# Kernel optimization log

Measured on AMD Instinct MI355X. Metric: run time of the kernel, lower is better.

## Reference

```python
import jax, jax.numpy as jnp
import numpy as np

NENTITY = 100000
NRELATION = 500
HIDDEN = 256
GAMMA = 12.0
BATCH = 8


def setup_inputs() -> dict:
    key = jax.random.key(0)
    k1, k2, k3, k4 = jax.random.split(key, 4)
    entity_embedding = jax.random.normal(k1, (NENTITY, HIDDEN), dtype=jnp.float32)
    relation_embedding = jax.random.normal(k2, (NRELATION, HIDDEN), dtype=jnp.float32)
    positive_sample = jax.random.randint(k3, (BATCH, 3), 0, NRELATION, dtype=jnp.int64)
    negative_sample = jax.random.randint(k4, (BATCH, NENTITY), 0, NENTITY, dtype=jnp.int64)
    return {
        "entity_embedding": entity_embedding,
        "relation_embedding": relation_embedding,
        "positive_sample": positive_sample,
        "negative_sample": negative_sample,
    }


def reference(entity_embedding, relation_embedding, positive_sample, negative_sample):
    # 'tail-batch' mode of KGEModel.forward + TransE scoring.
    # head, relation come from the positive triple; tail is every negative candidate.
    head = entity_embedding[positive_sample[:, 0]][:, None, :]      # [B, 1, H]
    relation = relation_embedding[positive_sample[:, 1]][:, None, :]  # [B, 1, H]
    tail = entity_embedding[negative_sample]                          # [B, N, H]
    # score = gamma - || head + relation - tail ||_1
    score = GAMMA - jnp.sum(jnp.abs(head + relation - tail), axis=-1)  # [B, N]
    return score
```

## Files before the change

kernel.cpp:

```cpp
#include <hip/hip_runtime.h>

#define HIDDEN 256
#define GAMMA_F 12.0f
#define BATCH 8

__global__ __launch_bounds__(256) void kge_dist_kernel(
    const float* __restrict__ ent,
    const float* __restrict__ rel,
    const int*  __restrict__ pos,
    float* __restrict__ dist,
    int ngroups, int nent)
{
    const int lane = threadIdx.x & 63;
    const int r = lane >> 5;
    const int c = lane & 31;
    const int wave_gid = (blockIdx.x * 256 + threadIdx.x) >> 6;
    const int nwaves = gridDim.x * 4;

    float4 hrA[BATCH], hrB[BATCH];
    #pragma unroll
    for (int b = 0; b < BATCH; ++b) {
        const int hidx = pos[b * 3 + 0];
        const int ridx = pos[b * 3 + 1];
        const float* hrow = ent + (size_t)hidx * HIDDEN;
        const float* rrow = rel + (size_t)ridx * HIDDEN;
        float4 h = *(const float4*)(hrow + c * 4);
        float4 q = *(const float4*)(rrow + c * 4);
        hrA[b] = make_float4(h.x + q.x, h.y + q.y, h.z + q.z, h.w + q.w);
        h = *(const float4*)(hrow + 128 + c * 4);
        q = *(const float4*)(rrow + 128 + c * 4);
        hrB[b] = make_float4(h.x + q.x, h.y + q.y, h.z + q.z, h.w + q.w);
    }

    for (int grp = wave_gid; grp < ngroups; grp += nwaves) {
        const float* base = ent + (size_t)grp * 8 * HIDDEN;

        float4 tA[4], tB[4];
        #pragma unroll
        for (int j = 0; j < 4; ++j) {
            const float* rowb = base + (size_t)(2 * j + r) * HIDDEN;
            tA[j] = *(const float4*)(rowb + c * 4);
            tB[j] = *(const float4*)(rowb + 128 + c * 4);
        }

        float res = 0.0f;
        #pragma unroll
        for (int j = 0; j < 4; ++j) {
            float acc[BATCH];
            #pragma unroll
            for (int b = 0; b < BATCH; ++b) {
                acc[b] = fabsf(hrA[b].x - tA[j].x) + fabsf(hrA[b].y - tA[j].y)
                       + fabsf(hrA[b].z - tA[j].z) + fabsf(hrA[b].w - tA[j].w)
                       + fabsf(hrB[b].x - tB[j].x) + fabsf(hrB[b].y - tB[j].y)
                       + fabsf(hrB[b].z - tB[j].z) + fabsf(hrB[b].w - tB[j].w);
            }
            float v[4];
            {
                const bool p = lane & 1;
                #pragma unroll
                for (int k = 0; k < 4; ++k) {
                    const float keep = p ? acc[2 * k + 1] : acc[2 * k];
                    const float give = p ? acc[2 * k]     : acc[2 * k + 1];
                    v[k] = keep + __shfl_xor(give, 1, 64);
                }
            }
            float w2[2];
            {
                const bool p = (lane >> 1) & 1;
                #pragma unroll
                for (int k = 0; k < 2; ++k) {
                    const float keep = p ? v[2 * k + 1] : v[2 * k];
                    const float give = p ? v[2 * k]     : v[2 * k + 1];
                    w2[k] = keep + __shfl_xor(give, 2, 64);
                }
            }
            float s;
            {
                const bool p = (lane >> 2) & 1;
                const float keep = p ? w2[1] : w2[0];
                const float give = p ? w2[0] : w2[1];
                s = keep + __shfl_xor(give, 4, 64);
            }
            s += __shfl_xor(s, 8, 64);
            s += __shfl_xor(s, 16, 64);
            if (((lane >> 3) & 3) == j) res = GAMMA_F - s;
        }
        dist[(size_t)grp * 64 + ((lane >> 3) & 3) * 16 + r * 8 + (lane & 7)] = res;
    }

    if (wave_gid == 0) {
        for (int e = ngroups * 8; e < nent; ++e) {
            const float* rowb = ent + (size_t)e * HIDDEN;
            const float4 uA = *(const float4*)(rowb + c * 4);
            const float4 uB = *(const float4*)(rowb + 128 + c * 4);
            float acc[BATCH];
            #pragma unroll
            for (int b = 0; b < BATCH; ++b) {
                acc[b] = fabsf(hrA[b].x - uA.x) + fabsf(hrA[b].y - uA.y)
                       + fabsf(hrA[b].z - uA.z) + fabsf(hrA[b].w - uA.w)
                       + fabsf(hrB[b].x - uB.x) + fabsf(hrB[b].y - uB.y)
                       + fabsf(hrB[b].z - uB.z) + fabsf(hrB[b].w - uB.w);
            }
            float v[4];
            {
                const bool p = lane & 1;
                #pragma unroll
                for (int k = 0; k < 4; ++k) {
                    const float keep = p ? acc[2 * k + 1] : acc[2 * k];
                    const float give = p ? acc[2 * k]     : acc[2 * k + 1];
                    v[k] = keep + __shfl_xor(give, 1, 64);
                }
            }
            float w2[2];
            {
                const bool p = (lane >> 1) & 1;
                #pragma unroll
                for (int k = 0; k < 2; ++k) {
                    const float keep = p ? v[2 * k + 1] : v[2 * k];
                    const float give = p ? v[2 * k]     : v[2 * k + 1];
                    w2[k] = keep + __shfl_xor(give, 2, 64);
                }
            }
            float s;
            {
                const bool p = (lane >> 2) & 1;
                const float keep = p ? w2[1] : w2[0];
                const float give = p ? w2[0] : w2[1];
                s = keep + __shfl_xor(give, 4, 64);
            }
            s += __shfl_xor(s, 8, 64);
            s += __shfl_xor(s, 16, 64);
            if (lane < BATCH) dist[(size_t)e * BATCH + lane] = GAMMA_F - s;
        }
    }
}

__global__ __launch_bounds__(256) void kge_gather_kernel(
    const int*  __restrict__ neg,
    const float* __restrict__ dist,
    float* __restrict__ out,
    int nneg)
{
    const int b = blockIdx.y;
    const int n = (blockIdx.x * 256 + threadIdx.x) * 2;
    if (n + 1 < nneg) {
        const int2 idx = *(const int2*)(neg + (size_t)b * nneg + n);
        float2 r;
        r.x = dist[(size_t)idx.x * BATCH + b];
        r.y = dist[(size_t)idx.y * BATCH + b];
        *(float2*)(out + (size_t)b * nneg + n) = r;
    } else if (n < nneg) {
        out[(size_t)b * nneg + n] =
            dist[(size_t)neg[(size_t)b * nneg + n] * BATCH + b];
    }
}

extern "C" void kernel_launch(void* const* d_in, const int* in_sizes, int n_in,
                              void* d_out, int out_size, void* d_ws, size_t ws_size,
                              hipStream_t stream) {
    const float* ent = (const float*)d_in[0];
    const float* rel = (const float*)d_in[1];
    const int*   pos = (const int*)d_in[2];
    const int*   neg = (const int*)d_in[3];
    float* out = (float*)d_out;

    const int nent = in_sizes[0] / HIDDEN;
    const int nneg = in_sizes[3] / BATCH;
    float* dist = (float*)d_ws;

    const int ngroups = nent / 8;
    kge_dist_kernel<<<1024, 256, 0, stream>>>(ent, rel, pos, dist, ngroups, nent);

    const int npairs = (nneg + 1) / 2;
    dim3 gridB((npairs + 255) / 256, BATCH);
    kge_gather_kernel<<<gridB, 256, 0, stream>>>(neg, dist, out, nneg);
}
```

Baseline: 166.0 us.

## Double-buffer entity rows into LDS via direct global-to-LDS loads per wave

Replaces direct register loads of 8-row entity groups with per-wave double-buffered LDS staging of 4-row groups using global_load_lds, prefetching the next group while computing the current one. The goal is to hide global memory latency on the full entity-table stream. The change halves the group size, adds manual waitcnt management and 32KB of LDS per block, and relies on each wave reading only its own LDS slot without barriers.

```diff
diff --git a/kernel.cpp b/kernel.cpp
--- a/kernel.cpp
+++ b/kernel.cpp
@@ -3,19 +3,33 @@
 #define HIDDEN 256
 #define GAMMA_F 12.0f
 #define BATCH 8
-
-__global__ __launch_bounds__(256) void kge_dist_kernel(
+#define ROWS_PER_GRP 4
+#define GRP_FLOATS (ROWS_PER_GRP * HIDDEN)
+
+__device__ __forceinline__ void dma_row_16(const float* gsrc, float* ldst) {
+    __builtin_amdgcn_global_load_lds(
+        (const __attribute__((address_space(1))) unsigned int*)gsrc,
+        (__attribute__((address_space(3))) unsigned int*)ldst,
+        16, 0, 0);
+}
+
+#define WAITCNT_VM4 0xF74
+#define WAITCNT_VM0 0xF70
+
+__global__ __launch_bounds__(256, 4) void kge_dist_kernel(
     const float* __restrict__ ent,
     const float* __restrict__ rel,
     const int*  __restrict__ pos,
     float* __restrict__ dist,
-    int ngroups, int nent)
+    int ngroups, int nent, int nwaves)
 {
+    __shared__ float lds[4][2][GRP_FLOATS];
+
     const int lane = threadIdx.x & 63;
-    const int r = lane >> 5;
+    const int wslot = threadIdx.x >> 6;
+    const int r_ = lane >> 5;
     const int c = lane & 31;
     const int wave_gid = (blockIdx.x * 256 + threadIdx.x) >> 6;
-    const int nwaves = gridDim.x * 4;
 
     float4 hrA[BATCH], hrB[BATCH];
     #pragma unroll
@@ -32,64 +46,85 @@
         hrB[b] = make_float4(h.x + q.x, h.y + q.y, h.z + q.z, h.w + q.w);
     }
 
-    for (int grp = wave_gid; grp < ngroups; grp += nwaves) {
-        const float* base = ent + (size_t)grp * 8 * HIDDEN;
-
-        float4 tA[4], tB[4];
+    __builtin_amdgcn_s_waitcnt(WAITCNT_VM0);
+
+    int g = wave_gid;
+    int p = 0;
+    if (g < ngroups) {
+        const float* base = ent + (size_t)g * GRP_FLOATS;
         #pragma unroll
-        for (int j = 0; j < 4; ++j) {
-            const float* rowb = base + (size_t)(2 * j + r) * HIDDEN;
-            tA[j] = *(const float4*)(rowb + c * 4);
-            tB[j] = *(const float4*)(rowb + 128 + c * 4);
+        for (int rr = 0; rr < ROWS_PER_GRP; ++rr)
+            dma_row_16(base + rr * HIDDEN + lane * 4, &lds[wslot][0][rr * HIDDEN]);
+    }
+
+    while (g < ngroups) {
+        const int gn = g + nwaves;
+        if (gn < ngroups) {
+            const float* base = ent + (size_t)gn * GRP_FLOATS;
+            #pragma unroll
+            for (int rr = 0; rr < ROWS_PER_GRP; ++rr)
+                dma_row_16(base + rr * HIDDEN + lane * 4,
+                           &lds[wslot][p ^ 1][rr * HIDDEN]);
+            __builtin_amdgcn_s_waitcnt(WAITCNT_VM4);
+        } else {
+            __builtin_amdgcn_s_waitcnt(WAITCNT_VM0);
         }
 
+        const float* buf = &lds[wslot][p][0];
         float res = 0.0f;
+        const int q = (lane >> 3) & 3;
         #pragma unroll
-        for (int j = 0; j < 4; ++j) {
+        for (int j = 0; j < 2; ++j) {
+            const float4 tA = *(const float4*)(buf + (2 * j + r_) * HIDDEN + c * 4);
+            const float4 tB = *(const float4*)(buf + (2 * j + r_) * HIDDEN + 128 + c * 4);
             float acc[BATCH];
             #pragma unroll
             for (int b = 0; b < BATCH; ++b) {
-                acc[b] = fabsf(hrA[b].x - tA[j].x) + fabsf(hrA[b].y - tA[j].y)
-                       + fabsf(hrA[b].z - tA[j].z) + fabsf(hrA[b].w - tA[j].w)
-                       + fabsf(hrB[b].x - tB[j].x) + fabsf(hrB[b].y - tB[j].y)
-                       + fabsf(hrB[b].z - tB[j].z) + fabsf(hrB[b].w - tB[j].w);
+                acc[b] = fabsf(hrA[b].x - tA.x) + fabsf(hrA[b].y - tA.y)
+                       + fabsf(hrA[b].z - tA.z) + fabsf(hrA[b].w - tA.w)
+                       + fabsf(hrB[b].x - tB.x) + fabsf(hrB[b].y - tB.y)
+                       + fabsf(hrB[b].z - tB.z) + fabsf(hrB[b].w - tB.w);
             }
             float v[4];
             {
-                const bool p = lane & 1;
+                const bool pb = lane & 1;
                 #pragma unroll
                 for (int k = 0; k < 4; ++k) {
-                    const float keep = p ? acc[2 * k + 1] : acc[2 * k];
-                    const float give = p ? acc[2 * k]     : acc[2 * k + 1];
+                    const float keep = pb ? acc[2 * k + 1] : acc[2 * k];
+                    const float give = pb ? acc[2 * k]     : acc[2 * k + 1];
                     v[k] = keep + __shfl_xor(give, 1, 64);
                 }
             }
             float w2[2];
             {
-                const bool p = (lane >> 1) & 1;
+                const bool pb = (lane >> 1) & 1;
                 #pragma unroll
                 for (int k = 0; k < 2; ++k) {
-                    const float keep = p ? v[2 * k + 1] : v[2 * k];
-                    const float give = p ? v[2 * k]     : v[2 * k + 1];
+                    const float keep = pb ? v[2 * k + 1] : v[2 * k];
+                    const float give = pb ? v[2 * k]     : v[2 * k + 1];
                     w2[k] = keep + __shfl_xor(give, 2, 64);
                 }
             }
             float s;
             {
-                const bool p = (lane >> 2) & 1;
-                const float keep = p ? w2[1] : w2[0];
-                const float give = p ? w2[0] : w2[1];
+                const bool pb = (lane >> 2) & 1;
+                const float keep = pb ? w2[1] : w2[0];
+                const float give = pb ? w2[0] : w2[1];
                 s = keep + __shfl_xor(give, 4, 64);
             }
             s += __shfl_xor(s, 8, 64);
             s += __shfl_xor(s, 16, 64);
-            if (((lane >> 3) & 3) == j) res = GAMMA_F - s;
+            if (q == j) res = GAMMA_F - s;
         }
-        dist[(size_t)grp * 64 + ((lane >> 3) & 3) * 16 + r * 8 + (lane & 7)] = res;
+        if (q < 2)
+            dist[(size_t)g * (ROWS_PER_GRP * BATCH) + q * 16 + r_ * 8 + (lane & 7)] = res;
+
+        p ^= 1;
+        g = gn;
     }
 
     if (wave_gid == 0) {
-        for (int e = ngroups * 8; e < nent; ++e) {
+        for (int e = ngroups * ROWS_PER_GRP; e < nent; ++e) {
             const float* rowb = ent + (size_t)e * HIDDEN;
             const float4 uA = *(const float4*)(rowb + c * 4);
             const float4 uB = *(const float4*)(rowb + 128 + c * 4);
@@ -103,29 +138,29 @@
             }
             float v[4];
             {
-                const bool p = lane & 1;
+                const bool pb = lane & 1;
                 #pragma unroll
                 for (int k = 0; k < 4; ++k) {
-                    const float keep = p ? acc[2 * k + 1] : acc[2 * k];
-                    const float give = p ? acc[2 * k]     : acc[2 * k + 1];
+                    const float keep = pb ? acc[2 * k + 1] : acc[2 * k];
+                    const float give = pb ? acc[2 * k]     : acc[2 * k + 1];
                     v[k] = keep + __shfl_xor(give, 1, 64);
                 }
             }
             float w2[2];
             {
-                const bool p = (lane >> 1) & 1;
+                const bool pb = (lane >> 1) & 1;
                 #pragma unroll
                 for (int k = 0; k < 2; ++k) {
-                    const float keep = p ? v[2 * k + 1] : v[2 * k];
-                    const float give = p ? v[2 * k]     : v[2 * k + 1];
+                    const float keep = pb ? v[2 * k + 1] : v[2 * k];
+                    const float give = pb ? v[2 * k]     : v[2 * k + 1];
                     w2[k] = keep + __shfl_xor(give, 2, 64);
                 }
             }
             float s;
             {
-                const bool p = (lane >> 2) & 1;
-                const float keep = p ? w2[1] : w2[0];
-                const float give = p ? w2[0] : w2[1];
+                const bool pb = (lane >> 2) & 1;
+                const float keep = pb ? w2[1] : w2[0];
+                const float give = pb ? w2[0] : w2[1];
                 s = keep + __shfl_xor(give, 4, 64);
             }
             s += __shfl_xor(s, 8, 64);
@@ -168,8 +203,11 @@
     const int nneg = in_sizes[3] / BATCH;
     float* dist = (float*)d_ws;
 
-    const int ngroups = nent / 8;
-    kge_dist_kernel<<<1024, 256, 0, stream>>>(ent, rel, pos, dist, ngroups, nent);
+    const int ngroups = nent / ROWS_PER_GRP;
+    const int nblocks = 1024;
+    const int nwaves = nblocks * 4;
+    kge_dist_kernel<<<nblocks, 256, 0, stream>>>(ent, rel, pos, dist,
+                                                 ngroups, nent, nwaves);
 
     const int npairs = (nneg + 1) / 2;
     dim3 gridB((npairs + 255) / 256, BATCH);
```

New measurement: 166.3 us. About the same (+0.2%).
